# Kernel tuning notes

Measured on AMD Instinct MI355X. Metric: run time of the kernel, lower is better.

## Reference

```python
import jax, jax.numpy as jnp
import numpy as np

T, B, OBS, H, A = 1024, 512, 64, 128, 16


def setup_inputs() -> dict:
    key = jax.random.key(0)
    ks = jax.random.split(key, 20)
    s = lambda fan_in: 1.0 / np.sqrt(fan_in)
    return {
        "hidden": jnp.zeros((B, H), jnp.float32),
        "obs": jax.random.normal(ks[0], (T, B, OBS), jnp.float32),
        "dones": jax.random.bernoulli(ks[1], 0.05, (T, B)),
        # embedding Dense
        "W_emb": jax.random.normal(ks[2], (OBS, H), jnp.float32) * s(OBS),
        "b_emb": jnp.zeros((H,), jnp.float32),
        # GRUCell: input kernels (r|z|n) with bias, hidden kernels (r|z|n), only n-gate hidden bias
        "Wi": jax.random.normal(ks[3], (H, 3 * H), jnp.float32) * s(H),
        "bi": jnp.zeros((3 * H,), jnp.float32),
        "Wh": jax.random.normal(ks[4], (H, 3 * H), jnp.float32) * s(H),
        "bh_n": jnp.zeros((H,), jnp.float32),
        # actor head
        "Wa1": jax.random.normal(ks[5], (H, H), jnp.float32) * s(H),
        "ba1": jnp.zeros((H,), jnp.float32),
        "Wa2": jax.random.normal(ks[6], (H, A), jnp.float32) * (0.01 * s(H)),
        "ba2": jnp.zeros((A,), jnp.float32),
        # critic head
        "Wc1": jax.random.normal(ks[7], (H, H), jnp.float32) * s(H),
        "bc1": jnp.zeros((H,), jnp.float32),
        "Wc2": jax.random.normal(ks[8], (H, 1), jnp.float32) * s(H),
        "bc2": jnp.zeros((1,), jnp.float32),
    }


def reference(hidden, obs, dones, W_emb, b_emb, Wi, bi, Wh, bh_n,
              Wa1, ba1, Wa2, ba2, Wc1, bc1, Wc2, bc2):
    # embedding: Dense + relu, applied to all timesteps at once  [T,B,H]
    emb = jax.nn.relu(jnp.einsum("tbo,oh->tbh", obs, W_emb) + b_emb)
    # precompute input-side gate projections for all steps  [T,B,3H]
    xi = jnp.einsum("tbh,hg->tbg", emb, Wi) + bi

    def step(h, xs):
        xi_t, done_t = xs
        h = jnp.where(done_t[:, None], 0.0, h)  # reset carry on done
        hh = h @ Wh  # [B,3H]
        xr, xz, xn = jnp.split(xi_t, 3, axis=-1)
        hr, hz, hn = jnp.split(hh, 3, axis=-1)
        r = jax.nn.sigmoid(xr + hr)
        z = jax.nn.sigmoid(xz + hz)
        n = jnp.tanh(xn + r * (hn + bh_n))
        h_new = (1.0 - z) * n + z * h
        return h_new, h_new

    hidden, y = jax.lax.scan(step, hidden, (xi, dones))  # y: [T,B,H]

    # actor head -> categorical logits [T,B,A]
    a1 = jax.nn.relu(jnp.einsum("tbh,hk->tbk", y, Wa1) + ba1)
    logits = jnp.einsum("tbh,ha->tba", a1, Wa2) + ba2
    # critic head -> value [T,B]
    c1 = jax.nn.relu(jnp.einsum("tbh,hk->tbk", y, Wc1) + bc1)
    v = jnp.squeeze(jnp.einsum("tbh,hk->tbk", c1, Wc2) + bc2, axis=-1)
    return (hidden, logits, v)
```

## Files before the change

### kernel.cpp

```cpp
#include <hip/hip_runtime.h>

#define T_DIM 1024
#define B_DIM 512
#define OBS_DIM 64
#define H_DIM 128
#define G3 384
#define A_DIM 16
#define CT 256
#define NCHUNK 4

typedef __bf16 bf16;
typedef __attribute__((ext_vector_type(4))) __bf16 bf16x4;
typedef __attribute__((ext_vector_type(8))) __bf16 bf16x8;
typedef __attribute__((ext_vector_type(4))) float f32x4;

#define MFMA(a, b, c) __builtin_amdgcn_mfma_f32_16x16x32_bf16((a), (b), (c), 0, 0, 0)

__device__ __forceinline__ float sigm(float x) { return 1.0f / (1.0f + __expf(-x)); }
__device__ __forceinline__ float tanh_f(float x) { return 1.0f - 2.0f / (__expf(2.0f * x) + 1.0f); }

__global__ __launch_bounds__(256) void prep_k(
    const float* __restrict__ hidden, const int* __restrict__ dones,
    const float* __restrict__ W_emb, const float* __restrict__ Wi,
    const float* __restrict__ Wh, const float* __restrict__ Wa1,
    const float* __restrict__ Wa2, const float* __restrict__ Wc1,
    const float* __restrict__ Wc2,
    bf16* __restrict__ wembT, bf16* __restrict__ wiT, bf16* __restrict__ whT,
    bf16* __restrict__ wa1T, bf16* __restrict__ wa2T, bf16* __restrict__ wc1T,
    bf16* __restrict__ wc2T, float* __restrict__ h_state) {
  int i = blockIdx.x * 256 + threadIdx.x;
  if (i < 8192) { int n = i / OBS_DIM, k = i % OBS_DIM; wembT[i] = (bf16)W_emb[k * H_DIM + n]; return; }
  i -= 8192;
  if (i < 49152) { int g = i / H_DIM, k = i % H_DIM; wiT[i] = (bf16)Wi[k * G3 + g]; return; }
  i -= 49152;
  if (i < 49152) { int g = i / H_DIM, k = i % H_DIM; whT[i] = (bf16)Wh[k * G3 + g]; return; }
  i -= 49152;
  if (i < 16384) { int n = i / H_DIM, k = i % H_DIM; wa1T[i] = (bf16)Wa1[k * H_DIM + n]; return; }
  i -= 16384;
  if (i < 2048) { int a = i / H_DIM, k = i % H_DIM; wa2T[i] = (bf16)Wa2[k * A_DIM + a]; return; }
  i -= 2048;
  if (i < 16384) { int n = i / H_DIM, k = i % H_DIM; wc1T[i] = (bf16)Wc1[k * H_DIM + n]; return; }
  i -= 16384;
  if (i < 2048) { int r = i / H_DIM, k = i % H_DIM; wc2T[i] = (r == 0) ? (bf16)Wc2[k] : (bf16)0.0f; return; }
  i -= 2048;
  if (i < 65536) { int b = i / H_DIM; h_state[i] = dones[b] ? 0.0f : hidden[i]; return; }
}


__device__ __forceinline__ void phase1_body(
    char* smem, int bid, const float* __restrict__ obs,
    const float* __restrict__ b_emb, const float* __restrict__ bi,
    const bf16* __restrict__ wembT, const bf16* __restrict__ wiT,
    bf16* __restrict__ xi, int row_base) {
  bf16 (*obs_lds)[72]  = (bf16(*)[72])smem;
  bf16 (*emb_lds)[136] = (bf16(*)[136])(smem + 2304);
  bf16 (*strip)[392]   = (bf16(*)[392])(smem + 6656);
  int tid = threadIdx.x, wave = tid >> 6, lane = tid & 63;
  int nl = lane & 15, q = lane >> 4;

  bf16x8 we[2][2], wi_f[6][4];
  float bev[2], biv[6];
#pragma unroll
  for (int e = 0; e < 2; ++e) {
    int nt = wave * 2 + e;
#pragma unroll
    for (int kb = 0; kb < 2; ++kb)
      we[e][kb] = *(const bf16x8*)(wembT + (nt * 16 + nl) * OBS_DIM + kb * 32 + q * 8);
    bev[e] = b_emb[nt * 16 + nl];
  }
#pragma unroll
  for (int j = 0; j < 6; ++j) {
    int nt = wave * 6 + j;
#pragma unroll
    for (int kb = 0; kb < 4; ++kb)
      wi_f[j][kb] = *(const bf16x8*)(wiT + (nt * 16 + nl) * H_DIM + kb * 32 + q * 8);
    biv[j] = bi[nt * 16 + nl];
  }

  int srow = tid >> 4, scol = (tid & 15) * 4;
  for (int rt = 0; rt < 32; ++rt) {
    int r0 = bid * 512 + rt * 16;
    {
      const float* src = obs + ((long)row_base + r0 + srow) * OBS_DIM + scol;
      float4 vv = *(const float4*)src;
      bf16x4 b; b[0] = (bf16)vv.x; b[1] = (bf16)vv.y; b[2] = (bf16)vv.z; b[3] = (bf16)vv.w;
      *(bf16x4*)&obs_lds[srow][scol] = b;
    }
    __syncthreads();
    bf16x8 ao[2];
#pragma unroll
    for (int kb = 0; kb < 2; ++kb) ao[kb] = *(const bf16x8*)&obs_lds[nl][kb * 32 + q * 8];
#pragma unroll
    for (int e = 0; e < 2; ++e) {
      f32x4 c = {0.f, 0.f, 0.f, 0.f};
      c = MFMA(ao[0], we[e][0], c);
      c = MFMA(ao[1], we[e][1], c);
#pragma unroll
      for (int r = 0; r < 4; ++r) {
        float v = c[r] + bev[e];
        emb_lds[q * 4 + r][(wave * 2 + e) * 16 + nl] = (bf16)(v > 0.f ? v : 0.f);
      }
    }
    __syncthreads();
    bf16x8 ae[4];
#pragma unroll
    for (int kb = 0; kb < 4; ++kb) ae[kb] = *(const bf16x8*)&emb_lds[nl][kb * 32 + q * 8];
#pragma unroll
    for (int j = 0; j < 6; ++j) {
      int nt = wave * 6 + j;
      f32x4 c = {0.f, 0.f, 0.f, 0.f};
#pragma unroll
      for (int kb = 0; kb < 4; ++kb) c = MFMA(ae[kb], wi_f[j][kb], c);
      int gate = nt >> 3, dloc = (nt & 7) * 16 + nl;
      int pos = (gate < 2) ? (2 * dloc + gate) : (256 + dloc);
#pragma unroll
      for (int r = 0; r < 4; ++r) strip[q * 4 + r][pos] = (bf16)(c[r] + biv[j]);
    }
    __syncthreads();
    bf16* dst = xi + (long)r0 * G3;
#pragma unroll
    for (int it = 0; it < 3; ++it) {
      int e0 = (it * 256 + tid) * 8;
      int row = e0 / G3, col = e0 % G3;
      *(int4*)(dst + e0) = *(const int4*)&strip[row][col];
    }
  }
}

__device__ __forceinline__ void scan_body(
    char* smem, int bid, const bf16* __restrict__ xi,
    const int* __restrict__ dones, const float* __restrict__ bh_n,
    const bf16* __restrict__ whT, float* __restrict__ h_state,
    bf16* __restrict__ y, float* __restrict__ hidden_out, int chunk) {
  bf16 (*hb)[2][136]       = (bf16(*)[2][136])smem;
  bf16 (*xibuf)[8][2][400] = (bf16(*)[8][2][400])(smem + 1088);
  int  (*dn)[2]            = (int(*)[2])(smem + 26688);

  __builtin_amdgcn_s_setprio(1);

  int tid = threadIdx.x;
  int wave = tid >> 6, lane = tid & 63;
  int nl = lane & 15, q = lane >> 4;
  int b0 = bid * 2;
  int ch = q & 1;
  int hsel = q >> 1;
  int dim = wave * 16 + (hsel << 6) + nl;
  int hrow = nl & 1;

  for (int i = tid; i <= CT; i += 256) {
    int t = chunk * CT + i;
    dn[i][0] = (t < T_DIM) ? dones[t * B_DIM + b0] : 0;
    dn[i][1] = (t < T_DIM) ? dones[t * B_DIM + b0 + 1] : 0;
  }
  int c0 = tid, c1 = 256 + tid, c2 = 512 + tid;
  int t0 = c0 / 96, p0 = c0 % 96, sc0 = p0 / 48, o0 = (p0 % 48) * 8;
  int t1 = c1 / 96, p1 = c1 % 96, sc1 = p1 / 48, o1 = (p1 % 48) * 8;
  int t2 = c2 / 96, p2 = c2 % 96, sc2 = p2 / 48, o2 = (p2 % 48) * 8;
  const long PSTR = (long)8 * B_DIM * G3;
  const bf16* pfs0 = xi + ((long)(8 + t0) * B_DIM + b0 + sc0) * G3 + o0;
  const bf16* pfs1 = xi + ((long)(8 + t1) * B_DIM + b0 + sc1) * G3 + o1;
  const bf16* pfs2 = xi + ((long)(8 + t2) * B_DIM + b0 + sc2) * G3 + o2;
  *(int4*)&xibuf[0][t0][sc0][o0] = *(const int4*)(xi + ((long)t0 * B_DIM + b0 + sc0) * G3 + o0);
  *(int4*)&xibuf[0][t1][sc1][o1] = *(const int4*)(xi + ((long)t1 * B_DIM + b0 + sc1) * G3 + o1);
  *(int4*)&xibuf[0][t2][sc2][o2] = *(const int4*)(xi + ((long)t2 * B_DIM + b0 + sc2) * G3 + o2);

  float hprev = h_state[(b0 + ch) * H_DIM + dim];
  hb[0][ch][dim] = (bf16)hprev;

  bf16x8 wf[6][4];
#pragma unroll
  for (int g = 0; g < 3; ++g)
#pragma unroll
    for (int hI = 0; hI < 2; ++hI)
#pragma unroll
      for (int kb = 0; kb < 4; ++kb)
        wf[g * 2 + hI][kb] =
            *(const bf16x8*)(whT + ((g * 8 + wave + 4 * hI) * 16 + nl) * H_DIM + kb * 32 + q * 8);
  float bhn = bh_n[dim];
  bf16* yp = y + (long)(b0 + ch) * H_DIM + dim;
  __syncthreads();

  int4 pfr0, pfr1, pfr2;

#define BAR()                                                                  \
  do {                                                                         \
    asm volatile("s_waitcnt lgkmcnt(0)" ::: "memory");                         \
    __builtin_amdgcn_sched_barrier(0);                                         \
    __builtin_amdgcn_s_barrier();                                              \
    __builtin_amdgcn_sched_barrier(0);                                         \
  } while (0)

#define MSTEP(HA, KB)                                                          \
  do {                                                                         \
    c0_ = MFMA(HA, wf[0][KB], c0_); c1_ = MFMA(HA, wf[1][KB], c1_);            \
    c2_ = MFMA(HA, wf[2][KB], c2_); c3_ = MFMA(HA, wf[3][KB], c3_);            \
    c4_ = MFMA(HA, wf[4][KB], c4_); c5_ = MFMA(HA, wf[5][KB], c5_);            \
  } while (0)

#define GSTEP(CUR, TS, TB, PF)                                                 \
  do {                                                                         \
    const int p_ = (TS) & 1;                                                   \
    bf16x8 ha0 = *(const bf16x8*)&hb[p_][hrow][0 * 32 + q * 8];                \
    bf16x8 ha1 = *(const bf16x8*)&hb[p_][hrow][1 * 32 + q * 8];                \
    bf16x8 ha2 = *(const bf16x8*)&hb[p_][hrow][2 * 32 + q * 8];                \
    bf16x8 ha3 = *(const bf16x8*)&hb[p_][hrow][3 * 32 + q * 8];                \
    const bf16* xrow_ = &xibuf[CUR][TS][ch][0];                                \
    unsigned urz_ = *(const unsigned*)(xrow_ + 2 * dim);                       \
    float xnv_ = (float)xrow_[256 + dim];                                      \
    int dnv_ = dn[(TB) + (TS) + 1][ch];                                        \
    if ((TS) == 0 && (PF)) {                                                   \
      pfr0 = *(const int4*)pfs0; pfs0 += PSTR;                                 \
      pfr1 = *(const int4*)pfs1; pfs1 += PSTR;                                 \
      pfr2 = *(const int4*)pfs2; pfs2 += PSTR;                                 \
    }                                                                          \
    f32x4 c0_ = {0.f, 0.f, 0.f, 0.f}, c1_ = {0.f, 0.f, 0.f, 0.f};             \
    f32x4 c2_ = {0.f, 0.f, 0.f, 0.f}, c3_ = {0.f, 0.f, 0.f, 0.f};             \
    f32x4 c4_ = {0.f, 0.f, 0.f, 0.f}, c5_ = {0.f, 0.f, 0.f, 0.f};             \
    MSTEP(ha0, 0); MSTEP(ha1, 1); MSTEP(ha2, 2); MSTEP(ha3, 3);                \
    if ((TS) == 7 && (PF)) {                                                   \
      *(int4*)&xibuf[(CUR) ^ 1][t0][sc0][o0] = pfr0;                           \
      *(int4*)&xibuf[(CUR) ^ 1][t1][sc1][o1] = pfr1;                           \
      *(int4*)&xibuf[(CUR) ^ 1][t2][sc2][o2] = pfr2;                           \
    }                                                                          \
    float hr_ = hsel ? (ch ? c1_[1] : c1_[0]) : (ch ? c0_[1] : c0_[0]);        \
    float hz_ = hsel ? (ch ? c3_[1] : c3_[0]) : (ch ? c2_[1] : c2_[0]);        \
    float hn_ = hsel ? (ch ? c5_[1] : c5_[0]) : (ch ? c4_[1] : c4_[0]);        \
    union { unsigned u; float f; } cvr_, cvz_;                                 \
    cvr_.u = urz_ << 16; cvz_.u = urz_ & 0xffff0000u;                          \
    float r_ = sigm(cvr_.f + hr_);                                             \
    float z_ = sigm(cvz_.f + hz_);                                             \
    float n_ = tanh_f(xnv_ + r_ * (hn_ + bhn));                                \
    float hnew_ = (1.0f - z_) * n_ + z_ * hprev;                               \
    float heff_ = dnv_ ? 0.0f : hnew_;                                         \
    *yp = (bf16)hnew_; yp += B_DIM * H_DIM;                                    \
    hb[p_ ^ 1][ch][dim] = (bf16)heff_;                                         \
    hprev = heff_;                                                             \
    BAR();                                                                     \
  } while (0)

  for (int tb = 0; tb < CT; tb += 16) {
    GSTEP(0, 0, tb, 1); GSTEP(0, 1, tb, 1); GSTEP(0, 2, tb, 1); GSTEP(0, 3, tb, 1);
    GSTEP(0, 4, tb, 1); GSTEP(0, 5, tb, 1); GSTEP(0, 6, tb, 1); GSTEP(0, 7, tb, 1);
    const int pfB = (tb + 16 < CT) ? 1 : 0;
    GSTEP(1, 0, tb + 8, pfB); GSTEP(1, 1, tb + 8, pfB); GSTEP(1, 2, tb + 8, pfB);
    GSTEP(1, 3, tb + 8, pfB); GSTEP(1, 4, tb + 8, pfB); GSTEP(1, 5, tb + 8, pfB);
    GSTEP(1, 6, tb + 8, pfB); GSTEP(1, 7, tb + 8, pfB);
  }
#undef GSTEP
#undef MSTEP
#undef BAR
  __builtin_amdgcn_s_setprio(0);

  h_state[(b0 + ch) * H_DIM + dim] = hprev;
  if (chunk == NCHUNK - 1) hidden_out[(b0 + ch) * H_DIM + dim] = hprev;
}

__device__ __forceinline__ void heads_body(
    char* smem, int bid, const bf16* __restrict__ y,
    const float* __restrict__ ba1, const float* __restrict__ ba2,
    const float* __restrict__ bc1, const float* __restrict__ bc2,
    const bf16* __restrict__ wa1T, const bf16* __restrict__ wa2T,
    const bf16* __restrict__ wc1T, const bf16* __restrict__ wc2T,
    float* __restrict__ logits, float* __restrict__ v, int t_base) {
  bf16  (*y_lds)[136] = (bf16(*)[136])smem;
  bf16  (*a1s)[136]   = (bf16(*)[136])(smem + 4352);
  bf16  (*c1s)[136]   = (bf16(*)[136])(smem + 8704);
  float (*s_o)[16]    = (float(*)[16])(smem + 13056);
  float (*s_v)        = (float*)(smem + 14080);
  int tid = threadIdx.x, wave = tid >> 6, lane = tid & 63;
  int nl = lane & 15, q = lane >> 4;

  bf16x8 wa1f[2][4], wc1f[2][4], wa2f[4], wc2f[4];
  float ba1v[2], bc1v[2];
#pragma unroll
  for (int e = 0; e < 2; ++e) {
    int nt = wave * 2 + e;
#pragma unroll
    for (int kb = 0; kb < 4; ++kb) {
      wa1f[e][kb] = *(const bf16x8*)(wa1T + (nt * 16 + nl) * H_DIM + kb * 32 + q * 8);
      wc1f[e][kb] = *(const bf16x8*)(wc1T + (nt * 16 + nl) * H_DIM + kb * 32 + q * 8);
    }
    ba1v[e] = ba1[nt * 16 + nl];
    bc1v[e] = bc1[nt * 16 + nl];
  }
#pragma unroll
  for (int kb = 0; kb < 4; ++kb) {
    wa2f[kb] = *(const bf16x8*)(wa2T + nl * H_DIM + kb * 32 + q * 8);
    wc2f[kb] = *(const bf16x8*)(wc2T + nl * H_DIM + kb * 32 + q * 8);
  }
  float ba2v = ba2[nl], bc2v = bc2[0];

  int srow = tid >> 4, scol = (tid & 15) * 8;
  for (int rt = 0; rt < 32; ++rt) {
    int r0 = bid * 512 + rt * 16;
    long gr0 = (long)t_base * B_DIM + r0;
    *(int4*)&y_lds[srow][scol] = *(const int4*)(y + (long)(r0 + srow) * H_DIM + scol);
    __syncthreads();
    bf16x8 ya[4];
#pragma unroll
    for (int kb = 0; kb < 4; ++kb) ya[kb] = *(const bf16x8*)&y_lds[nl][kb * 32 + q * 8];
#pragma unroll
    for (int e = 0; e < 2; ++e) {
      f32x4 ca = {0.f, 0.f, 0.f, 0.f}, cc = {0.f, 0.f, 0.f, 0.f};
#pragma unroll
      for (int kb = 0; kb < 4; ++kb) {
        ca = MFMA(ya[kb], wa1f[e][kb], ca);
        cc = MFMA(ya[kb], wc1f[e][kb], cc);
      }
      int colb = (wave * 2 + e) * 16 + nl;
#pragma unroll
      for (int r = 0; r < 4; ++r) {
        float va = ca[r] + ba1v[e];
        float vc = cc[r] + bc1v[e];
        a1s[q * 4 + r][colb] = (bf16)(va > 0.f ? va : 0.f);
        c1s[q * 4 + r][colb] = (bf16)(vc > 0.f ? vc : 0.f);
      }
    }
    __syncthreads();
    if (wave == 0) {
      bf16x8 a1f[4];
#pragma unroll
      for (int kb = 0; kb < 4; ++kb) a1f[kb] = *(const bf16x8*)&a1s[nl][kb * 32 + q * 8];
      f32x4 c = {0.f, 0.f, 0.f, 0.f};
#pragma unroll
      for (int kb = 0; kb < 4; ++kb) c = MFMA(a1f[kb], wa2f[kb], c);
#pragma unroll
      for (int r = 0; r < 4; ++r) s_o[q * 4 + r][nl] = c[r] + ba2v;
    } else if (wave == 1) {
      bf16x8 c1f[4];
#pragma unroll
      for (int kb = 0; kb < 4; ++kb) c1f[kb] = *(const bf16x8*)&c1s[nl][kb * 32 + q * 8];
      f32x4 c = {0.f, 0.f, 0.f, 0.f};
#pragma unroll
      for (int kb = 0; kb < 4; ++kb) c = MFMA(c1f[kb], wc2f[kb], c);
      if (nl == 0) {
#pragma unroll
        for (int r = 0; r < 4; ++r) s_v[q * 4 + r] = c[r] + bc2v;
      }
    }
    __syncthreads();
    if (tid < 64) {
      *(int4*)(logits + gr0 * A_DIM + tid * 4) = *(const int4*)&s_o[tid >> 2][(tid & 3) * 4];
    } else if (tid < 80) {
      v[gr0 + (tid - 64)] = s_v[tid - 64];
    }
  }
}

__global__ __launch_bounds__(256, 3) void fused_k(
    const float* __restrict__ obs, const float* __restrict__ b_emb,
    const float* __restrict__ bi, const bf16* __restrict__ wembT,
    const bf16* __restrict__ wiT, bf16* __restrict__ xi0, bf16* __restrict__ xi1,
    const int* __restrict__ dones, const float* __restrict__ bh_n,
    const bf16* __restrict__ whT, float* __restrict__ h_state,
    bf16* __restrict__ y0, bf16* __restrict__ y1, float* __restrict__ hidden_out,
    const float* __restrict__ ba1, const float* __restrict__ ba2,
    const float* __restrict__ bc1, const float* __restrict__ bc2,
    const bf16* __restrict__ wa1T, const bf16* __restrict__ wa2T,
    const bf16* __restrict__ wc1T, const bf16* __restrict__ wc2T,
    float* __restrict__ logits, float* __restrict__ v, int cs) {
  __shared__ __align__(16) char smem[50176];
  int bid = blockIdx.x;
  if (bid < 256) {
    if (cs >= 0 && cs < NCHUNK)
      scan_body(smem, bid, (cs & 1) ? xi1 : xi0, dones, bh_n, whT, h_state,
                (cs & 1) ? y1 : y0, hidden_out, cs);
    return;
  }
  if (bid < 512) {
    int cp = cs + 1;
    if (cp >= 0 && cp < NCHUNK)
      phase1_body(smem, bid - 256, obs, b_emb, bi, wembT, wiT,
                  (cp & 1) ? xi1 : xi0, cp * CT * B_DIM);
    return;
  }
  {
    int ch2 = cs - 1;
    if (ch2 >= 0 && ch2 < NCHUNK)
      heads_body(smem, bid - 512, (ch2 & 1) ? y1 : y0, ba1, ba2, bc1, bc2,
                 wa1T, wa2T, wc1T, wc2T, logits, v, ch2 * CT);
  }
}

extern "C" void kernel_launch(void* const* d_in, const int* in_sizes, int n_in,
                              void* d_out, int out_size, void* d_ws, size_t ws_size,
                              hipStream_t stream) {
  const float* hidden = (const float*)d_in[0];
  const float* obs    = (const float*)d_in[1];
  const int*   dones  = (const int*)d_in[2];
  const float* W_emb  = (const float*)d_in[3];
  const float* b_emb  = (const float*)d_in[4];
  const float* Wi     = (const float*)d_in[5];
  const float* bi     = (const float*)d_in[6];
  const float* Wh     = (const float*)d_in[7];
  const float* bh_n   = (const float*)d_in[8];
  const float* Wa1    = (const float*)d_in[9];
  const float* ba1    = (const float*)d_in[10];
  const float* Wa2    = (const float*)d_in[11];
  const float* ba2    = (const float*)d_in[12];
  const float* Wc1    = (const float*)d_in[13];
  const float* bc1    = (const float*)d_in[14];
  const float* Wc2    = (const float*)d_in[15];
  const float* bc2    = (const float*)d_in[16];

  float* out_hidden = (float*)d_out;
  float* out_logits = out_hidden + B_DIM * H_DIM;
  float* out_v      = out_logits + (long)T_DIM * B_DIM * A_DIM;

  char* ws = (char*)d_ws;
  bf16*  wembT   = (bf16*)(ws + 0);
  bf16*  wiT     = (bf16*)(ws + 16384);
  bf16*  whT     = (bf16*)(ws + 114688);
  bf16*  wa1T    = (bf16*)(ws + 212992);
  bf16*  wa2T    = (bf16*)(ws + 245760);
  bf16*  wc1T    = (bf16*)(ws + 249856);
  bf16*  wc2T    = (bf16*)(ws + 282624);
  float* h_state = (float*)(ws + 286720);
  bf16*  xi0     = (bf16*)(ws + 548864);
  bf16*  xi1     = (bf16*)(ws + 101212160);
  bf16*  y0      = (bf16*)(ws + 201875456);
  bf16*  y1      = (bf16*)(ws + 235429888);

  prep_k<<<816, 256, 0, stream>>>(hidden, dones, W_emb, Wi, Wh, Wa1, Wa2, Wc1, Wc2,
                                  wembT, wiT, whT, wa1T, wa2T, wc1T, wc2T, h_state);
  for (int cs = -1; cs <= NCHUNK; ++cs) {
    fused_k<<<768, 256, 0, stream>>>(obs, b_emb, bi, wembT, wiT, xi0, xi1,
                                     dones, bh_n, whT, h_state, y0, y1, out_hidden,
                                     ba1, ba2, bc1, bc2, wa1T, wa2T, wc1T, wc2T,
                                     out_logits, out_v, cs);
  }
  (void)in_sizes; (void)n_in; (void)out_size; (void)ws_size;
}
```

Before: 910.6 us.

## Merge phase1 and heads into shared blocks and spread edge launches across grid

Shrinks the fused launch grid from 768 to 512 blocks. The non-scan blocks now run both the next chunk's input projection and the previous chunk's heads one after the other, instead of using separate block ranges. The first and last launches (prologue phase1 only, epilogue heads only) now spread their work across all 512 blocks with 16 tiles each, so fewer CTAs sit idle. Launch bounds drop to 2 blocks per CU, and trailing syncs are added so LDS can be reused safely between phases; the trade is that these blocks run their phases serially.

```diff
diff --git a/kernel.cpp b/kernel.cpp
--- a/kernel.cpp
+++ b/kernel.cpp
@@ -48,7 +48,7 @@
 
 
 __device__ __forceinline__ void phase1_body(
-    char* smem, int bid, const float* __restrict__ obs,
+    char* smem, int tile_base, int ntiles, const float* __restrict__ obs,
     const float* __restrict__ b_emb, const float* __restrict__ bi,
     const bf16* __restrict__ wembT, const bf16* __restrict__ wiT,
     bf16* __restrict__ xi, int row_base) {
@@ -78,8 +78,8 @@
   }
 
   int srow = tid >> 4, scol = (tid & 15) * 4;
-  for (int rt = 0; rt < 32; ++rt) {
-    int r0 = bid * 512 + rt * 16;
+  for (int rt = 0; rt < ntiles; ++rt) {
+    int r0 = (tile_base + rt) * 16;
     {
       const float* src = obs + ((long)row_base + r0 + srow) * OBS_DIM + scol;
       float4 vv = *(const float4*)src;
@@ -124,6 +124,7 @@
       int row = e0 / G3, col = e0 % G3;
       *(int4*)(dst + e0) = *(const int4*)&strip[row][col];
     }
+    __syncthreads();
   }
 }
 
@@ -256,7 +257,7 @@
 }
 
 __device__ __forceinline__ void heads_body(
-    char* smem, int bid, const bf16* __restrict__ y,
+    char* smem, int tile_base, int ntiles, const bf16* __restrict__ y,
     const float* __restrict__ ba1, const float* __restrict__ ba2,
     const float* __restrict__ bc1, const float* __restrict__ bc2,
     const bf16* __restrict__ wa1T, const bf16* __restrict__ wa2T,
@@ -291,8 +292,8 @@
   float ba2v = ba2[nl], bc2v = bc2[0];
 
   int srow = tid >> 4, scol = (tid & 15) * 8;
-  for (int rt = 0; rt < 32; ++rt) {
-    int r0 = bid * 512 + rt * 16;
+  for (int rt = 0; rt < ntiles; ++rt) {
+    int r0 = (tile_base + rt) * 16;
     long gr0 = (long)t_base * B_DIM + r0;
     *(int4*)&y_lds[srow][scol] = *(const int4*)(y + (long)(r0 + srow) * H_DIM + scol);
     __syncthreads();
@@ -344,10 +345,11 @@
     } else if (tid < 80) {
       v[gr0 + (tid - 64)] = s_v[tid - 64];
     }
-  }
-}
-
-__global__ __launch_bounds__(256, 3) void fused_k(
+    __syncthreads();
+  }
+}
+
+__global__ __launch_bounds__(256, 2) void fused_k(
     const float* __restrict__ obs, const float* __restrict__ b_emb,
     const float* __restrict__ bi, const bf16* __restrict__ wembT,
     const bf16* __restrict__ wiT, bf16* __restrict__ xi0, bf16* __restrict__ xi1,
@@ -361,23 +363,29 @@
     float* __restrict__ logits, float* __restrict__ v, int cs) {
   __shared__ __align__(16) char smem[50176];
   int bid = blockIdx.x;
+  if (cs == -1) {
+    phase1_body(smem, bid * 16, 16, obs, b_emb, bi, wembT, wiT, xi0, 0);
+    return;
+  }
+  if (cs == NCHUNK) {
+    heads_body(smem, bid * 16, 16, ((NCHUNK - 1) & 1) ? y1 : y0, ba1, ba2, bc1,
+               bc2, wa1T, wa2T, wc1T, wc2T, logits, v, (NCHUNK - 1) * CT);
+    return;
+  }
   if (bid < 256) {
-    if (cs >= 0 && cs < NCHUNK)
-      scan_body(smem, bid, (cs & 1) ? xi1 : xi0, dones, bh_n, whT, h_state,
-                (cs & 1) ? y1 : y0, hidden_out, cs);
+    scan_body(smem, bid, (cs & 1) ? xi1 : xi0, dones, bh_n, whT, h_state,
+              (cs & 1) ? y1 : y0, hidden_out, cs);
     return;
   }
-  if (bid < 512) {
+  {
+    int wb = bid - 256;
     int cp = cs + 1;
-    if (cp >= 0 && cp < NCHUNK)
-      phase1_body(smem, bid - 256, obs, b_emb, bi, wembT, wiT,
+    if (cp < NCHUNK)
+      phase1_body(smem, wb * 32, 32, obs, b_emb, bi, wembT, wiT,
                   (cp & 1) ? xi1 : xi0, cp * CT * B_DIM);
-    return;
-  }
-  {
     int ch2 = cs - 1;
-    if (ch2 >= 0 && ch2 < NCHUNK)
-      heads_body(smem, bid - 512, (ch2 & 1) ? y1 : y0, ba1, ba2, bc1, bc2,
+    if (ch2 >= 0)
+      heads_body(smem, wb * 32, 32, (ch2 & 1) ? y1 : y0, ba1, ba2, bc1, bc2,
                  wa1T, wa2T, wc1T, wc2T, logits, v, ch2 * CT);
   }
 }
@@ -424,7 +432,7 @@
   prep_k<<<816, 256, 0, stream>>>(hidden, dones, W_emb, Wi, Wh, Wa1, Wa2, Wc1, Wc2,
                                   wembT, wiT, whT, wa1T, wa2T, wc1T, wc2T, h_state);
   for (int cs = -1; cs <= NCHUNK; ++cs) {
-    fused_k<<<768, 256, 0, stream>>>(obs, b_emb, bi, wembT, wiT, xi0, xi1,
+    fused_k<<<512, 256, 0, stream>>>(obs, b_emb, bi, wembT, wiT, xi0, xi1,
                                      dones, bh_n, whT, h_state, y0, y1, out_hidden,
                                      ba1, ba2, bc1, bc2, wa1T, wa2T, wc1T, wc2T,
                                      out_logits, out_v, cs);
```

Result: faster. 748.1 us (-17.8%).
